# Optimization experiments

Hardware: AMD Instinct MI355X
Metric: run time of the kernel (lower is better)

## Reference

```python
import jax, jax.numpy as jnp
import numpy as np

N, E, D_IN, D_H, D_OUT, L = 100000, 1000000, 128, 64, 40, 7
MSG_EPS = 1e-7   # GENConv message epsilon
BN_EPS = 1e-5    # torch BatchNorm1d eps
T = 1.0          # softmax temperature (learn_t=False)


def _segment_softmax(logits, seg, n):
    # numerically stable softmax over edges grouped by destination node
    m = jax.ops.segment_max(logits, seg, num_segments=n)
    e = jnp.exp(logits - m[seg])
    s = jax.ops.segment_sum(e, seg, num_segments=n)
    return e / (s[seg] + 1e-16)


def _gen_conv(h, src, dst, W, b):
    # GENConv, aggr='softmax_sg', mlp_layers=1, msg_norm=False
    msg = jax.nn.relu(h[src]) + MSG_EPS                 # [E, D_H]
    w = jax.lax.stop_gradient(_segment_softmax(msg * T, dst, N))
    agg = jax.ops.segment_sum(w * msg, dst, num_segments=N)  # [N, D_H]
    return (h + agg) @ W + b


def _batch_norm(h, gamma, beta):
    mu = jnp.mean(h, axis=0)
    var = jnp.mean(jnp.square(h - mu), axis=0)  # biased var (training mode)
    return gamma * (h - mu) * jax.lax.rsqrt(var + BN_EPS) + beta


def setup_inputs() -> dict:
    key = jax.random.key(0)
    ks = jax.random.split(key, 6)
    x = jax.random.normal(ks[0], (N, D_IN), dtype=jnp.float32)
    edge_index = jax.random.randint(ks[1], (2, E), 0, N, dtype=jnp.int64)
    W_enc = jax.random.normal(ks[2], (D_IN, D_H), dtype=jnp.float32) / np.float32(np.sqrt(D_IN))
    b_enc = jnp.zeros((D_H,), jnp.float32)
    Wg = jax.random.normal(ks[3], (L, D_H, D_H), dtype=jnp.float32) / np.float32(np.sqrt(D_H))
    bg = jnp.zeros((L, D_H), jnp.float32)
    gamma = jnp.ones((L, D_H), jnp.float32)
    beta = jnp.zeros((L, D_H), jnp.float32)
    W_pred = jax.random.normal(ks[4], (D_H, D_OUT), dtype=jnp.float32) / np.float32(np.sqrt(D_H))
    b_pred = jnp.zeros((D_OUT,), jnp.float32)
    return {"x": x, "edge_index": edge_index, "W_enc": W_enc, "b_enc": b_enc,
            "Wg": Wg, "bg": bg, "gamma": gamma, "beta": beta,
            "W_pred": W_pred, "b_pred": b_pred}


def reference(x, edge_index, W_enc, b_enc, Wg, bg, gamma, beta, W_pred, b_pred):
    src, dst = edge_index[0], edge_index[1]
    h = x @ W_enc + b_enc                               # node encoder
    h = _gen_conv(h, src, dst, Wg[0], bg[0])            # first conv (res+)
    for layer in range(1, L):                            # BN->ReLU->Conv->Res
        h2 = jax.nn.relu(_batch_norm(h, gamma[layer - 1], beta[layer - 1]))
        h = _gen_conv(h2, src, dst, Wg[layer], bg[layer]) + h
    h = jax.nn.relu(_batch_norm(h, gamma[L - 1], beta[L - 1]))
    logits = h @ W_pred + b_pred
    return jax.nn.log_softmax(logits, axis=-1)
```

## Files before the change

kernel.cpp:

```cpp
#include <hip/hip_runtime.h>
#include <math.h>

#define NN 100000
#define NE 1000000
#define DH 64
#define DIN 128
#define DOUT 40
#define NL 7
#define SCAN_B 1024
#define NBLK ((NN + SCAN_B - 1) / SCAN_B)
#define NGRP (NN / 16)
#define LBLK ((NGRP + 3) / 4)
#define COLB_CAP (NE + 8 * NN + 64)
#define QS 16.0f
#define IQS 0.0625f

typedef _Float16 v8h __attribute__((ext_vector_type(8)));
typedef float v4f __attribute__((ext_vector_type(4)));

__global__ __launch_bounds__(256) void k_count4(const int* __restrict__ dst,
                                                int* __restrict__ cnt4,
                                                int* __restrict__ pi) {
  int i = blockIdx.x * 256 + threadIdx.x;
  if (i < NE) pi[i] = atomicAdd(&cnt4[(size_t)(i & 3) * NN + dst[i]], 1);
}

__global__ __launch_bounds__(SCAN_B) void k_scan1(const int* __restrict__ cnt4,
                                                  int* __restrict__ cnt,
                                                  int* __restrict__ rp8,
                                                  int* __restrict__ rp8s,
                                                  int* __restrict__ bsum) {
  __shared__ int buf[SCAN_B];
  int i = blockIdx.x * SCAN_B + threadIdx.x;
  int c0 = 0, c1 = 0, c2 = 0, c3 = 0;
  if (i < NN) {
    c0 = cnt4[i];
    c1 = cnt4[(size_t)NN + i];
    c2 = cnt4[(size_t)2 * NN + i];
    c3 = cnt4[(size_t)3 * NN + i];
  }
  int tot = c0 + c1 + c2 + c3;
  int t8 = (tot + 7) & ~7;
  buf[threadIdx.x] = t8;
  __syncthreads();
  for (int off = 1; off < SCAN_B; off <<= 1) {
    int t = (threadIdx.x >= off) ? buf[threadIdx.x - off] : 0;
    __syncthreads();
    buf[threadIdx.x] += t;
    __syncthreads();
  }
  if (i < NN) {
    int excl = buf[threadIdx.x] - t8;
    cnt[i] = tot;
    rp8[i] = excl;
    rp8s[4 * i] = excl;
    rp8s[4 * i + 1] = excl + c0;
    rp8s[4 * i + 2] = excl + c0 + c1;
    rp8s[4 * i + 3] = excl + c0 + c1 + c2;
  }
  if (threadIdx.x == SCAN_B - 1) bsum[blockIdx.x] = buf[SCAN_B - 1];
}

__global__ __launch_bounds__(128) void k_scan2(int* __restrict__ bsum) {
  __shared__ int buf[128];
  int v = (threadIdx.x < NBLK) ? bsum[threadIdx.x] : 0;
  buf[threadIdx.x] = v;
  __syncthreads();
  for (int off = 1; off < 128; off <<= 1) {
    int t = (threadIdx.x >= off) ? buf[threadIdx.x - off] : 0;
    __syncthreads();
    buf[threadIdx.x] += t;
    __syncthreads();
  }
  if (threadIdx.x < NBLK) bsum[threadIdx.x] = buf[threadIdx.x] - v;
}

__global__ __launch_bounds__(SCAN_B) void k_scan3(int* __restrict__ rp8,
                                                  int* __restrict__ rp8s,
                                                  const int* __restrict__ bsum) {
  int i = blockIdx.x * SCAN_B + threadIdx.x;
  if (i < NN) {
    int b = bsum[blockIdx.x];
    rp8[i] += b;
    rp8s[4 * i] += b;
    rp8s[4 * i + 1] += b;
    rp8s[4 * i + 2] += b;
    rp8s[4 * i + 3] += b;
  }
}

__global__ __launch_bounds__(256) void k_place(const int* __restrict__ src,
                                               const int* __restrict__ dst,
                                               const int* __restrict__ rp8s,
                                               const int* __restrict__ pi,
                                               int* __restrict__ colb) {
  int i = blockIdx.x * 256 + threadIdx.x;
  if (i < NE)
    colb[rp8s[4 * dst[i] + (i & 3)] + pi[i]] = src[i] * DH + DH;
}

__global__ __launch_bounds__(256) void k_enc_mfma(const float* __restrict__ x,
                                                  const float* __restrict__ W,
                                                  const float* __restrict__ b,
                                                  float* __restrict__ h) {
  __shared__ _Float16 Atile[4][2048];
  const int tid = threadIdx.x;
  const int w = tid >> 6, lane = tid & 63;
  const int gid = blockIdx.x * 4 + w;
  if (gid >= NGRP) return;
  const int row = lane & 15, hi = lane >> 4;

  v8h bf[4][4];
#pragma unroll
  for (int kt = 0; kt < 4; ++kt)
#pragma unroll
    for (int ct = 0; ct < 4; ++ct)
#pragma unroll
      for (int j = 0; j < 8; ++j)
        bf[kt][ct][j] = (_Float16)W[(kt * 32 + hi * 8 + j) * DH + ct * 16 + row];

  const int base = gid * 16;
  _Float16* At = &Atile[w][0];
#pragma unroll 4
  for (int i = 0; i < 16; ++i) {
    float v0 = x[(size_t)(base + i) * DIN + lane];
    float v1 = x[(size_t)(base + i) * DIN + 64 + lane];
    int swi = (i & 7) << 4;
    At[(i * 256 + ((lane * 2) ^ swi)) >> 1] = (_Float16)v0;
    At[(i * 256 + 128 + ((lane * 2) ^ swi)) >> 1] = (_Float16)v1;
  }
  const int sw = (row & 7) << 4;
  v8h a[4];
#pragma unroll
  for (int kt = 0; kt < 4; ++kt) {
    int off = (kt & 1) * 64 + hi * 16;
    a[kt] = *(const v8h*)&At[(row * 256 + (kt >> 1) * 128 + (off ^ sw)) >> 1];
  }
  v4f c0 = {0, 0, 0, 0}, c1 = {0, 0, 0, 0}, c2 = {0, 0, 0, 0}, c3 = {0, 0, 0, 0};
#pragma unroll
  for (int kt = 0; kt < 4; ++kt) {
    c0 = __builtin_amdgcn_mfma_f32_16x16x32_f16(a[kt], bf[kt][0], c0, 0, 0, 0);
    c1 = __builtin_amdgcn_mfma_f32_16x16x32_f16(a[kt], bf[kt][1], c1, 0, 0, 0);
    c2 = __builtin_amdgcn_mfma_f32_16x16x32_f16(a[kt], bf[kt][2], c2, 0, 0, 0);
    c3 = __builtin_amdgcn_mfma_f32_16x16x32_f16(a[kt], bf[kt][3], c3, 0, 0, 0);
  }
  float b0 = b[row], b1 = b[16 + row], b2 = b[32 + row], b3 = b[48 + row];
#pragma unroll
  for (int reg = 0; reg < 4; ++reg) {
    size_t o = (size_t)(base + hi * 4 + reg) * DH;
    h[o + row] = c0[reg] + b0;
    h[o + 16 + row] = c1[reg] + b1;
    h[o + 32 + row] = c2[reg] + b2;
    h[o + 48 + row] = c3[reg] + b3;
  }
}

__global__ __launch_bounds__(256) void k_msg(const float* __restrict__ h,
                                             const float* __restrict__ stats_in,
                                             const float* __restrict__ gamma,
                                             const float* __restrict__ beta,
                                             unsigned char* __restrict__ msg) {
  int lane = threadIdx.x & 63;
  float scale = 1.f, shift = 0.f;
  if (stats_in) {
    float mu = stats_in[lane] * (1.0f / NN);
    float var = stats_in[64 + lane] * (1.0f / NN) - mu * mu;
    scale = gamma[lane] * rsqrtf(var + 1e-5f);
    shift = beta[lane] - mu * scale;
  }
  int wid = (blockIdx.x * blockDim.x + threadIdx.x) >> 6;
  int nw = (gridDim.x * blockDim.x) >> 6;
  for (int n = wid; n < NN; n += nw) {
    float r = h[n * DH + lane];
    float v = fmaxf(fmaf(r, scale, shift), 0.f) + 1e-7f;
    msg[DH + n * DH + lane] = (unsigned char)fminf(v * QS + 0.5f, 255.f);
  }
}

__global__ __launch_bounds__(256, 8) void k_agg(const unsigned char* __restrict__ msg,
                                                const int* __restrict__ rp8,
                                                const int* __restrict__ cnt,
                                                const int* __restrict__ colb,
                                                _Float16* __restrict__ agg) {
  const int lane = threadIdx.x & 63;
  const int n = (blockIdx.x * 256 + threadIdx.x) >> 6;
  const int beg = __builtin_amdgcn_readfirstlane(rp8[n]);
  const int deg = __builtin_amdgcn_readfirstlane(cnt[n]);
  const int pdeg = (deg + 7) & ~7;
  const unsigned char* mb = msg + lane;
  float s = 0.f, t = 0.f;
  for (int j = 0; j < pdeg; j += 8) {
    int cc[8];
#pragma unroll
    for (int k = 0; k < 8; ++k) cc[k] = colb[beg + j + k];
    float vv[8];
#pragma unroll
    for (int k = 0; k < 8; ++k) vv[k] = (float)mb[cc[k]] * IQS;
#pragma unroll
    for (int k = 0; k < 8; ++k) {
      float e = __expf(vv[k]);
      s += e;
      t = fmaf(e, vv[k], t);
    }
  }
  s -= (float)(pdeg - deg);
  agg[(size_t)n * DH + lane] = (_Float16)(t / (s + 1e-16f));
}

__global__ __launch_bounds__(256) void k_mfma(
    const float* __restrict__ h_pre, const _Float16* __restrict__ agg,
    const float* __restrict__ stats_in,
    const float* __restrict__ gamma, const float* __restrict__ beta,
    const float* __restrict__ W, const float* __restrict__ b, int add_res,
    float* __restrict__ hout, float* __restrict__ partial) {
  __shared__ _Float16 Atile[4][1024];
  const int tid = threadIdx.x;
  const int w = tid >> 6, lane = tid & 63;
  const int gid = blockIdx.x * 4 + w;
  const int row = lane & 15, hi = lane >> 4;

  float ss0 = 0, ss1 = 0, ss2 = 0, ss3 = 0;
  float qq0 = 0, qq1 = 0, qq2 = 0, qq3 = 0;

  if (gid < NGRP) {
    float scale = 1.f, shift = 0.f;
    if (stats_in) {
      float mu = stats_in[lane] * (1.0f / NN);
      float var = stats_in[64 + lane] * (1.0f / NN) - mu * mu;
      scale = gamma[lane] * rsqrtf(var + 1e-5f);
      shift = beta[lane] - mu * scale;
    }
    v8h bf[2][4];
#pragma unroll
    for (int kt = 0; kt < 2; ++kt)
#pragma unroll
      for (int ct = 0; ct < 4; ++ct)
#pragma unroll
        for (int j = 0; j < 8; ++j)
          bf[kt][ct][j] = (_Float16)W[(kt * 32 + hi * 8 + j) * DH + ct * 16 + row];

    const int base = gid * 16;
    const float* hl = h_pre + lane;
    const _Float16* agl = agg + lane;
    _Float16* At = &Atile[w][0];

    float rawv[16], agv[16];
#pragma unroll
    for (int i = 0; i < 16; ++i) {
      size_t o = (size_t)(base + i) * DH;
      rawv[i] = hl[o];
      agv[i] = (float)agl[o];
    }
    float res[4][4];
    if (add_res) {
#pragma unroll
      for (int reg = 0; reg < 4; ++reg) {
        size_t o = (size_t)(base + hi * 4 + reg) * DH;
        res[reg][0] = h_pre[o + row];
        res[reg][1] = h_pre[o + 16 + row];
        res[reg][2] = h_pre[o + 32 + row];
        res[reg][3] = h_pre[o + 48 + row];
      }
    }
#pragma unroll
    for (int i = 0; i < 16; ++i) {
      float v = stats_in ? fmaxf(fmaf(rawv[i], scale, shift), 0.f) : rawv[i];
      v += agv[i];
      At[(i * 128 + ((lane * 2) ^ ((i & 7) << 4))) >> 1] = (_Float16)v;
    }
    const int sw = (row & 7) << 4;
    v8h a0 = *(const v8h*)&At[((row * 128) + ((hi * 16) ^ sw)) >> 1];
    v8h a1 = *(const v8h*)&At[((row * 128) + ((64 + hi * 16) ^ sw)) >> 1];
    v4f c0 = {0, 0, 0, 0}, c1 = {0, 0, 0, 0}, c2 = {0, 0, 0, 0}, c3 = {0, 0, 0, 0};
    c0 = __builtin_amdgcn_mfma_f32_16x16x32_f16(a0, bf[0][0], c0, 0, 0, 0);
    c0 = __builtin_amdgcn_mfma_f32_16x16x32_f16(a1, bf[1][0], c0, 0, 0, 0);
    c1 = __builtin_amdgcn_mfma_f32_16x16x32_f16(a0, bf[0][1], c1, 0, 0, 0);
    c1 = __builtin_amdgcn_mfma_f32_16x16x32_f16(a1, bf[1][1], c1, 0, 0, 0);
    c2 = __builtin_amdgcn_mfma_f32_16x16x32_f16(a0, bf[0][2], c2, 0, 0, 0);
    c2 = __builtin_amdgcn_mfma_f32_16x16x32_f16(a1, bf[1][2], c2, 0, 0, 0);
    c3 = __builtin_amdgcn_mfma_f32_16x16x32_f16(a0, bf[0][3], c3, 0, 0, 0);
    c3 = __builtin_amdgcn_mfma_f32_16x16x32_f16(a1, bf[1][3], c3, 0, 0, 0);

    float b0 = b[row], b1 = b[16 + row], b2 = b[32 + row], b3 = b[48 + row];
#pragma unroll
    for (int reg = 0; reg < 4; ++reg) {
      size_t o = (size_t)(base + hi * 4 + reg) * DH;
      float a0v = c0[reg] + b0;
      float a1v = c1[reg] + b1;
      float a2v = c2[reg] + b2;
      float a3v = c3[reg] + b3;
      if (add_res) {
        a0v += res[reg][0];
        a1v += res[reg][1];
        a2v += res[reg][2];
        a3v += res[reg][3];
      }
      hout[o + row] = a0v;
      hout[o + 16 + row] = a1v;
      hout[o + 32 + row] = a2v;
      hout[o + 48 + row] = a3v;
      ss0 += a0v; qq0 = fmaf(a0v, a0v, qq0);
      ss1 += a1v; qq1 = fmaf(a1v, a1v, qq1);
      ss2 += a2v; qq2 = fmaf(a2v, a2v, qq2);
      ss3 += a3v; qq3 = fmaf(a3v, a3v, qq3);
    }
  }

#pragma unroll
  for (int off = 16; off <= 32; off <<= 1) {
    ss0 += __shfl_xor(ss0, off, 64); ss1 += __shfl_xor(ss1, off, 64);
    ss2 += __shfl_xor(ss2, off, 64); ss3 += __shfl_xor(ss3, off, 64);
    qq0 += __shfl_xor(qq0, off, 64); qq1 += __shfl_xor(qq1, off, 64);
    qq2 += __shfl_xor(qq2, off, 64); qq3 += __shfl_xor(qq3, off, 64);
  }
  __syncthreads();
  float* Sr = (float*)&Atile[0][0];
  if (lane < 16) {
    Sr[w * 128 + lane] = ss0;       Sr[w * 128 + 16 + lane] = ss1;
    Sr[w * 128 + 32 + lane] = ss2;  Sr[w * 128 + 48 + lane] = ss3;
    Sr[w * 128 + 64 + lane] = qq0;  Sr[w * 128 + 80 + lane] = qq1;
    Sr[w * 128 + 96 + lane] = qq2;  Sr[w * 128 + 112 + lane] = qq3;
  }
  __syncthreads();
  if (tid < 128) {
    float vsum = Sr[tid] + Sr[128 + tid] + Sr[256 + tid] + Sr[384 + tid];
    partial[(size_t)blockIdx.x * 128 + tid] = vsum;
  }
}

__global__ __launch_bounds__(256) void k_red(const float* __restrict__ partial,
                                             float* __restrict__ stats) {
  const int f = blockIdx.x;
  float acc = 0.f;
  for (int i = threadIdx.x; i < LBLK; i += 256)
    acc += partial[(size_t)i * 128 + f];
  __shared__ float buf[256];
  buf[threadIdx.x] = acc;
  __syncthreads();
  for (int off = 128; off >= 1; off >>= 1) {
    if (threadIdx.x < off) buf[threadIdx.x] += buf[threadIdx.x + off];
    __syncthreads();
  }
  if (threadIdx.x == 0) stats[f] = buf[0];
}

__global__ __launch_bounds__(256) void k_pred_mfma(
    const float* __restrict__ h_pre, const float* __restrict__ stats_in,
    const float* __restrict__ gamma, const float* __restrict__ beta,
    const float* __restrict__ Wp, const float* __restrict__ bp,
    float* __restrict__ out) {
  __shared__ _Float16 Atile[4][1024];
  const int tid = threadIdx.x;
  const int w = tid >> 6, lane = tid & 63;
  const int gid = blockIdx.x * 4 + w;
  if (gid >= NGRP) return;
  const int row = lane & 15, hi = lane >> 4;

  float mu = stats_in[lane] * (1.0f / NN);
  float var = stats_in[64 + lane] * (1.0f / NN) - mu * mu;
  float scale = gamma[lane] * rsqrtf(var + 1e-5f);
  float shift = beta[lane] - mu * scale;

  v8h bf[2][3];
#pragma unroll
  for (int kt = 0; kt < 2; ++kt)
#pragma unroll
    for (int ct = 0; ct < 3; ++ct) {
      int n = ct * 16 + row;
#pragma unroll
      for (int j = 0; j < 8; ++j)
        bf[kt][ct][j] =
            (n < DOUT) ? (_Float16)Wp[(kt * 32 + hi * 8 + j) * DOUT + n]
                       : (_Float16)0.f;
    }

  const int base = gid * 16;
  const float* hl = h_pre + lane;
  _Float16* At = &Atile[w][0];
#pragma unroll 4
  for (int i = 0; i < 16; ++i) {
    float raw = hl[(size_t)(base + i) * DH];
    float v = fmaxf(fmaf(raw, scale, shift), 0.f);
    At[(i * 128 + ((lane * 2) ^ ((i & 7) << 4))) >> 1] = (_Float16)v;
  }
  const int sw = (row & 7) << 4;
  v8h a0 = *(const v8h*)&At[((row * 128) + ((hi * 16) ^ sw)) >> 1];
  v8h a1 = *(const v8h*)&At[((row * 128) + ((64 + hi * 16) ^ sw)) >> 1];
  v4f c0 = {0, 0, 0, 0}, c1 = {0, 0, 0, 0}, c2 = {0, 0, 0, 0};
  c0 = __builtin_amdgcn_mfma_f32_16x16x32_f16(a0, bf[0][0], c0, 0, 0, 0);
  c0 = __builtin_amdgcn_mfma_f32_16x16x32_f16(a1, bf[1][0], c0, 0, 0, 0);
  c1 = __builtin_amdgcn_mfma_f32_16x16x32_f16(a0, bf[0][1], c1, 0, 0, 0);
  c1 = __builtin_amdgcn_mfma_f32_16x16x32_f16(a1, bf[1][1], c1, 0, 0, 0);
  c2 = __builtin_amdgcn_mfma_f32_16x16x32_f16(a0, bf[0][2], c2, 0, 0, 0);
  c2 = __builtin_amdgcn_mfma_f32_16x16x32_f16(a1, bf[1][2], c2, 0, 0, 0);

  float bp0 = bp[row], bp1 = bp[16 + row];
  float bp2 = (32 + row < DOUT) ? bp[32 + row] : 0.f;
  bool v2 = (32 + row) < DOUT;
#pragma unroll
  for (int reg = 0; reg < 4; ++reg) {
    float l0 = c0[reg] + bp0;
    float l1 = c1[reg] + bp1;
    float l2 = v2 ? (c2[reg] + bp2) : -INFINITY;
    float xm = fmaxf(fmaxf(l0, l1), l2);
#pragma unroll
    for (int off = 1; off <= 8; off <<= 1) xm = fmaxf(xm, __shfl_xor(xm, off, 64));
    float e = __expf(l0 - xm) + __expf(l1 - xm) + (v2 ? __expf(l2 - xm) : 0.f);
#pragma unroll
    for (int off = 1; off <= 8; off <<= 1) e += __shfl_xor(e, off, 64);
    float ls = xm + __logf(e);
    size_t o = (size_t)(base + hi * 4 + reg) * DOUT;
    out[o + row] = l0 - ls;
    out[o + 16 + row] = l1 - ls;
    if (v2) out[o + 32 + row] = l2 - ls;
  }
}

extern "C" void kernel_launch(void* const* d_in, const int* in_sizes, int n_in,
                              void* d_out, int out_size, void* d_ws, size_t ws_size,
                              hipStream_t stream) {
  const float* x      = (const float*)d_in[0];
  const int*   ei     = (const int*)d_in[1];
  const float* W_enc  = (const float*)d_in[2];
  const float* b_enc  = (const float*)d_in[3];
  const float* Wg     = (const float*)d_in[4];
  const float* bg     = (const float*)d_in[5];
  const float* gamma  = (const float*)d_in[6];
  const float* beta   = (const float*)d_in[7];
  const float* W_pred = (const float*)d_in[8];
  const float* b_pred = (const float*)d_in[9];
  float* out = (float*)d_out;

  const int* src = ei;
  const int* dst = ei + NE;

  char* p = (char*)d_ws;
  auto alloc = [&](size_t bytes) -> void* {
    void* r = (void*)p;
    p += (bytes + 255) & ~(size_t)255;
    return r;
  };
  float*         hA      = (float*)alloc((size_t)NN * DH * 4);
  float*         hB      = (float*)alloc((size_t)NN * DH * 4);
  unsigned char* msg     = (unsigned char*)alloc((size_t)(NN + 1) * DH);
  _Float16*      agg     = (_Float16*)alloc((size_t)NN * DH * 2);
  int*           rp8     = (int*)alloc((size_t)NN * 4);
  int*           rp8s    = (int*)alloc((size_t)NN * 4 * 4);
  int*           pi      = (int*)alloc((size_t)NE * 4);
  int*           cnt     = (int*)alloc((size_t)NN * 4);
  int*           cnt4    = (int*)alloc((size_t)NN * 4 * 4);
  int*           colb    = (int*)alloc((size_t)COLB_CAP * 4);
  int*           bsum    = (int*)alloc((size_t)NBLK * 4);
  float*         stats   = (float*)alloc((size_t)NL * 128 * 4);
  float*         partial = (float*)alloc((size_t)LBLK * 128 * 4);

  hipMemsetAsync(cnt4, 0, (size_t)NN * 16, stream);
  hipMemsetAsync(colb, 0, (size_t)COLB_CAP * 4, stream);
  hipMemsetAsync(msg, 0, DH, stream);

  k_count4<<<(NE + 255) / 256, 256, 0, stream>>>(dst, cnt4, pi);
  k_scan1<<<NBLK, SCAN_B, 0, stream>>>(cnt4, cnt, rp8, rp8s, bsum);
  k_scan2<<<1, 128, 0, stream>>>(bsum);
  k_scan3<<<NBLK, SCAN_B, 0, stream>>>(rp8, rp8s, bsum);
  k_place<<<(NE + 255) / 256, 256, 0, stream>>>(src, dst, rp8s, pi, colb);

  k_enc_mfma<<<LBLK, 256, 0, stream>>>(x, W_enc, b_enc, hA);

  const int MSG_BLOCKS = 1024;
  const int AGG_BLOCKS = NN * 64 / 256;

  k_msg<<<MSG_BLOCKS, 256, 0, stream>>>(hA, nullptr, nullptr, nullptr, msg);
  k_agg<<<AGG_BLOCKS, 256, 0, stream>>>(msg, rp8, cnt, colb, agg);
  k_mfma<<<LBLK, 256, 0, stream>>>(
      hA, agg, nullptr, nullptr, nullptr, Wg, bg, 0, hB, partial);
  k_red<<<128, 256, 0, stream>>>(partial, stats);

  float* h = hB;
  float* hn = hA;
  for (int l = 1; l < NL; ++l) {
    const float* st = stats + (size_t)(l - 1) * 128;
    const float* g  = gamma + (size_t)(l - 1) * DH;
    const float* be = beta + (size_t)(l - 1) * DH;
    k_msg<<<MSG_BLOCKS, 256, 0, stream>>>(h, st, g, be, msg);
    k_agg<<<AGG_BLOCKS, 256, 0, stream>>>(msg, rp8, cnt, colb, agg);
    k_mfma<<<LBLK, 256, 0, stream>>>(
        h, agg, st, g, be,
        Wg + (size_t)l * DH * DH, bg + (size_t)l * DH, 1,
        hn, partial);
    k_red<<<128, 256, 0, stream>>>(partial, stats + (size_t)l * 128);
    float* tmp = h; h = hn; hn = tmp;
  }

  k_pred_mfma<<<LBLK, 256, 0, stream>>>(
      h, stats + (size_t)(NL - 1) * 128,
      gamma + (size_t)(NL - 1) * DH, beta + (size_t)(NL - 1) * DH,
      W_pred, b_pred, out);
}
```

Baseline: 517.5 us.

## Fuse softmax aggregation into MFMA layer kernel, dropping the fp16 agg buffer

Merges the per-node softmax aggregation kernel and the MFMA linear/residual/stats kernel into one kernel. Each block handles 16 nodes: every wave aggregates 4 nodes, writes the combined input tile to shared memory, then computes one 16-column slice of the output with MFMA. This removes the agg round-trip through global memory and one launch per layer. In exchange each block now does more serial gather work per wave, every block loads its slice of W, and the partial-stats buffer and k_red's reduction grow to one entry per 16 nodes.

Measured after the change: 525.2 us. Within noise of the previous version (+1.5%).

```diff
diff --git a/kernel.cpp b/kernel.cpp
--- a/kernel.cpp
+++ b/kernel.cpp
@@ -177,154 +177,88 @@
   }
 }
 
-__global__ __launch_bounds__(256, 8) void k_agg(const unsigned char* __restrict__ msg,
-                                                const int* __restrict__ rp8,
-                                                const int* __restrict__ cnt,
-                                                const int* __restrict__ colb,
-                                                _Float16* __restrict__ agg) {
-  const int lane = threadIdx.x & 63;
-  const int n = (blockIdx.x * 256 + threadIdx.x) >> 6;
-  const int beg = __builtin_amdgcn_readfirstlane(rp8[n]);
-  const int deg = __builtin_amdgcn_readfirstlane(cnt[n]);
-  const int pdeg = (deg + 7) & ~7;
-  const unsigned char* mb = msg + lane;
-  float s = 0.f, t = 0.f;
-  for (int j = 0; j < pdeg; j += 8) {
-    int cc[8];
-#pragma unroll
-    for (int k = 0; k < 8; ++k) cc[k] = colb[beg + j + k];
-    float vv[8];
-#pragma unroll
-    for (int k = 0; k < 8; ++k) vv[k] = (float)mb[cc[k]] * IQS;
-#pragma unroll
-    for (int k = 0; k < 8; ++k) {
-      float e = __expf(vv[k]);
-      s += e;
-      t = fmaf(e, vv[k], t);
-    }
-  }
-  s -= (float)(pdeg - deg);
-  agg[(size_t)n * DH + lane] = (_Float16)(t / (s + 1e-16f));
-}
-
-__global__ __launch_bounds__(256) void k_mfma(
-    const float* __restrict__ h_pre, const _Float16* __restrict__ agg,
-    const float* __restrict__ stats_in,
+__global__ __launch_bounds__(256) void k_layer2(
+    const float* __restrict__ h_pre, const unsigned char* __restrict__ msg,
+    const int* __restrict__ rp8, const int* __restrict__ cnt,
+    const int* __restrict__ colb, const float* __restrict__ stats_in,
     const float* __restrict__ gamma, const float* __restrict__ beta,
     const float* __restrict__ W, const float* __restrict__ b, int add_res,
     float* __restrict__ hout, float* __restrict__ partial) {
-  __shared__ _Float16 Atile[4][1024];
+  __shared__ _Float16 At[1024];
   const int tid = threadIdx.x;
   const int w = tid >> 6, lane = tid & 63;
-  const int gid = blockIdx.x * 4 + w;
   const int row = lane & 15, hi = lane >> 4;
-
-  float ss0 = 0, ss1 = 0, ss2 = 0, ss3 = 0;
-  float qq0 = 0, qq1 = 0, qq2 = 0, qq3 = 0;
-
-  if (gid < NGRP) {
-    float scale = 1.f, shift = 0.f;
-    if (stats_in) {
-      float mu = stats_in[lane] * (1.0f / NN);
-      float var = stats_in[64 + lane] * (1.0f / NN) - mu * mu;
-      scale = gamma[lane] * rsqrtf(var + 1e-5f);
-      shift = beta[lane] - mu * scale;
-    }
-    v8h bf[2][4];
-#pragma unroll
-    for (int kt = 0; kt < 2; ++kt)
-#pragma unroll
-      for (int ct = 0; ct < 4; ++ct)
-#pragma unroll
-        for (int j = 0; j < 8; ++j)
-          bf[kt][ct][j] = (_Float16)W[(kt * 32 + hi * 8 + j) * DH + ct * 16 + row];
-
-    const int base = gid * 16;
-    const float* hl = h_pre + lane;
-    const _Float16* agl = agg + lane;
-    _Float16* At = &Atile[w][0];
-
-    float rawv[16], agv[16];
-#pragma unroll
-    for (int i = 0; i < 16; ++i) {
-      size_t o = (size_t)(base + i) * DH;
-      rawv[i] = hl[o];
-      agv[i] = (float)agl[o];
-    }
-    float res[4][4];
-    if (add_res) {
-#pragma unroll
-      for (int reg = 0; reg < 4; ++reg) {
-        size_t o = (size_t)(base + hi * 4 + reg) * DH;
-        res[reg][0] = h_pre[o + row];
-        res[reg][1] = h_pre[o + 16 + row];
-        res[reg][2] = h_pre[o + 32 + row];
-        res[reg][3] = h_pre[o + 48 + row];
+  const int base = blockIdx.x * 16;
+
+  float scale = 1.f, shift = 0.f;
+  if (stats_in) {
+    float mu = stats_in[lane] * (1.0f / NN);
+    float var = stats_in[64 + lane] * (1.0f / NN) - mu * mu;
+    scale = gamma[lane] * rsqrtf(var + 1e-5f);
+    shift = beta[lane] - mu * scale;
+  }
+  v8h bf0, bf1;
+#pragma unroll
+  for (int j = 0; j < 8; ++j) {
+    bf0[j] = (_Float16)W[(hi * 8 + j) * DH + w * 16 + row];
+    bf1[j] = (_Float16)W[(32 + hi * 8 + j) * DH + w * 16 + row];
+  }
+
+  const unsigned char* mb = msg + lane;
+#pragma unroll
+  for (int k = 0; k < 4; ++k) {
+    int n = base + w * 4 + k;
+    int beg = __builtin_amdgcn_readfirstlane(rp8[n]);
+    int deg = __builtin_amdgcn_readfirstlane(cnt[n]);
+    int pdeg = (deg + 7) & ~7;
+    float s = 0.f, t = 0.f;
+    for (int j = 0; j < pdeg; j += 8) {
+      int cc[8];
+#pragma unroll
+      for (int q = 0; q < 8; ++q) cc[q] = colb[beg + j + q];
+      float vv[8];
+#pragma unroll
+      for (int q = 0; q < 8; ++q) vv[q] = (float)mb[cc[q]] * IQS;
+#pragma unroll
+      for (int q = 0; q < 8; ++q) {
+        float e = __expf(vv[q]);
+        s += e;
+        t = fmaf(e, vv[q], t);
       }
     }
-#pragma unroll
-    for (int i = 0; i < 16; ++i) {
-      float v = stats_in ? fmaxf(fmaf(rawv[i], scale, shift), 0.f) : rawv[i];
-      v += agv[i];
-      At[(i * 128 + ((lane * 2) ^ ((i & 7) << 4))) >> 1] = (_Float16)v;
-    }
-    const int sw = (row & 7) << 4;
-    v8h a0 = *(const v8h*)&At[((row * 128) + ((hi * 16) ^ sw)) >> 1];
-    v8h a1 = *(const v8h*)&At[((row * 128) + ((64 + hi * 16) ^ sw)) >> 1];
-    v4f c0 = {0, 0, 0, 0}, c1 = {0, 0, 0, 0}, c2 = {0, 0, 0, 0}, c3 = {0, 0, 0, 0};
-    c0 = __builtin_amdgcn_mfma_f32_16x16x32_f16(a0, bf[0][0], c0, 0, 0, 0);
-    c0 = __builtin_amdgcn_mfma_f32_16x16x32_f16(a1, bf[1][0], c0, 0, 0, 0);
-    c1 = __builtin_amdgcn_mfma_f32_16x16x32_f16(a0, bf[0][1], c1, 0, 0, 0);
-    c1 = __builtin_amdgcn_mfma_f32_16x16x32_f16(a1, bf[1][1], c1, 0, 0, 0);
-    c2 = __builtin_amdgcn_mfma_f32_16x16x32_f16(a0, bf[0][2], c2, 0, 0, 0);
-    c2 = __builtin_amdgcn_mfma_f32_16x16x32_f16(a1, bf[1][2], c2, 0, 0, 0);
-    c3 = __builtin_amdgcn_mfma_f32_16x16x32_f16(a0, bf[0][3], c3, 0, 0, 0);
-    c3 = __builtin_amdgcn_mfma_f32_16x16x32_f16(a1, bf[1][3], c3, 0, 0, 0);
-
-    float b0 = b[row], b1 = b[16 + row], b2 = b[32 + row], b3 = b[48 + row];
-#pragma unroll
-    for (int reg = 0; reg < 4; ++reg) {
-      size_t o = (size_t)(base + hi * 4 + reg) * DH;
-      float a0v = c0[reg] + b0;
-      float a1v = c1[reg] + b1;
-      float a2v = c2[reg] + b2;
-      float a3v = c3[reg] + b3;
-      if (add_res) {
-        a0v += res[reg][0];
-        a1v += res[reg][1];
-        a2v += res[reg][2];
-        a3v += res[reg][3];
-      }
-      hout[o + row] = a0v;
-      hout[o + 16 + row] = a1v;
-      hout[o + 32 + row] = a2v;
-      hout[o + 48 + row] = a3v;
-      ss0 += a0v; qq0 = fmaf(a0v, a0v, qq0);
-      ss1 += a1v; qq1 = fmaf(a1v, a1v, qq1);
-      ss2 += a2v; qq2 = fmaf(a2v, a2v, qq2);
-      ss3 += a3v; qq3 = fmaf(a3v, a3v, qq3);
-    }
-  }
-
-#pragma unroll
-  for (int off = 16; off <= 32; off <<= 1) {
-    ss0 += __shfl_xor(ss0, off, 64); ss1 += __shfl_xor(ss1, off, 64);
-    ss2 += __shfl_xor(ss2, off, 64); ss3 += __shfl_xor(ss3, off, 64);
-    qq0 += __shfl_xor(qq0, off, 64); qq1 += __shfl_xor(qq1, off, 64);
-    qq2 += __shfl_xor(qq2, off, 64); qq3 += __shfl_xor(qq3, off, 64);
+    s -= (float)(pdeg - deg);
+    float aggv = t / (s + 1e-16f);
+    float raw = h_pre[(size_t)n * DH + lane];
+    float v = stats_in ? fmaxf(fmaf(raw, scale, shift), 0.f) : raw;
+    v += aggv;
+    int i = w * 4 + k;
+    At[(i * 128 + ((lane * 2) ^ ((i & 7) << 4))) >> 1] = (_Float16)v;
   }
   __syncthreads();
-  float* Sr = (float*)&Atile[0][0];
-  if (lane < 16) {
-    Sr[w * 128 + lane] = ss0;       Sr[w * 128 + 16 + lane] = ss1;
-    Sr[w * 128 + 32 + lane] = ss2;  Sr[w * 128 + 48 + lane] = ss3;
-    Sr[w * 128 + 64 + lane] = qq0;  Sr[w * 128 + 80 + lane] = qq1;
-    Sr[w * 128 + 96 + lane] = qq2;  Sr[w * 128 + 112 + lane] = qq3;
-  }
-  __syncthreads();
-  if (tid < 128) {
-    float vsum = Sr[tid] + Sr[128 + tid] + Sr[256 + tid] + Sr[384 + tid];
-    partial[(size_t)blockIdx.x * 128 + tid] = vsum;
+
+  const int sw = (row & 7) << 4;
+  v8h a0 = *(const v8h*)&At[((row * 128) + ((hi * 16) ^ sw)) >> 1];
+  v8h a1 = *(const v8h*)&At[((row * 128) + ((64 + hi * 16) ^ sw)) >> 1];
+  v4f c = {0, 0, 0, 0};
+  c = __builtin_amdgcn_mfma_f32_16x16x32_f16(a0, bf0, c, 0, 0, 0);
+  c = __builtin_amdgcn_mfma_f32_16x16x32_f16(a1, bf1, c, 0, 0, 0);
+
+  float bb = b[w * 16 + row];
+  float ss = 0.f, qq = 0.f;
+#pragma unroll
+  for (int reg = 0; reg < 4; ++reg) {
+    size_t o = (size_t)(base + hi * 4 + reg) * DH + w * 16 + row;
+    float av = c[reg] + bb;
+    if (add_res) av += h_pre[o];
+    hout[o] = av;
+    ss += av;
+    qq = fmaf(av, av, qq);
+  }
+  ss += __shfl_xor(ss, 16, 64); qq += __shfl_xor(qq, 16, 64);
+  ss += __shfl_xor(ss, 32, 64); qq += __shfl_xor(qq, 32, 64);
+  if (hi == 0) {
+    partial[(size_t)blockIdx.x * 128 + w * 16 + row] = ss;
+    partial[(size_t)blockIdx.x * 128 + 64 + w * 16 + row] = qq;
   }
 }
 
@@ -332,7 +266,7 @@
                                              float* __restrict__ stats) {
   const int f = blockIdx.x;
   float acc = 0.f;
-  for (int i = threadIdx.x; i < LBLK; i += 256)
+  for (int i = threadIdx.x; i < NGRP; i += 256)
     acc += partial[(size_t)i * 128 + f];
   __shared__ float buf[256];
   buf[threadIdx.x] = acc;
@@ -443,7 +377,6 @@
   float*         hA      = (float*)alloc((size_t)NN * DH * 4);
   float*         hB      = (float*)alloc((size_t)NN * DH * 4);
   unsigned char* msg     = (unsigned char*)alloc((size_t)(NN + 1) * DH);
-  _Float16*      agg     = (_Float16*)alloc((size_t)NN * DH * 2);
   int*           rp8     = (int*)alloc((size_t)NN * 4);
   int*           rp8s    = (int*)alloc((size_t)NN * 4 * 4);
   int*           pi      = (int*)alloc((size_t)NE * 4);
@@ -452,7 +385,7 @@
   int*           colb    = (int*)alloc((size_t)COLB_CAP * 4);
   int*           bsum    = (int*)alloc((size_t)NBLK * 4);
   float*         stats   = (float*)alloc((size_t)NL * 128 * 4);
-  float*         partial = (float*)alloc((size_t)LBLK * 128 * 4);
+  float*         partial = (float*)alloc((size_t)NGRP * 128 * 4);
 
   hipMemsetAsync(cnt4, 0, (size_t)NN * 16, stream);
   hipMemsetAsync(colb, 0, (size_t)COLB_CAP * 4, stream);
@@ -467,12 +400,10 @@
   k_enc_mfma<<<LBLK, 256, 0, stream>>>(x, W_enc, b_enc, hA);
 
   const int MSG_BLOCKS = 1024;
-  const int AGG_BLOCKS = NN * 64 / 256;
 
   k_msg<<<MSG_BLOCKS, 256, 0, stream>>>(hA, nullptr, nullptr, nullptr, msg);
-  k_agg<<<AGG_BLOCKS, 256, 0, stream>>>(msg, rp8, cnt, colb, agg);
-  k_mfma<<<LBLK, 256, 0, stream>>>(
-      hA, agg, nullptr, nullptr, nullptr, Wg, bg, 0, hB, partial);
+  k_layer2<<<NGRP, 256, 0, stream>>>(
+      hA, msg, rp8, cnt, colb, nullptr, nullptr, nullptr, Wg, bg, 0, hB, partial);
   k_red<<<128, 256, 0, stream>>>(partial, stats);
 
   float* h = hB;
@@ -482,9 +413,8 @@
     const float* g  = gamma + (size_t)(l - 1) * DH;
     const float* be = beta + (size_t)(l - 1) * DH;
     k_msg<<<MSG_BLOCKS, 256, 0, stream>>>(h, st, g, be, msg);
-    k_agg<<<AGG_BLOCKS, 256, 0, stream>>>(msg, rp8, cnt, colb, agg);
-    k_mfma<<<LBLK, 256, 0, stream>>>(
-        h, agg, st, g, be,
+    k_layer2<<<NGRP, 256, 0, stream>>>(
+        h, msg, rp8, cnt, colb, st, g, be,
         Wg + (size_t)l * DH * DH, bg + (size_t)l * DH, 1,
         hn, partial);
     k_red<<<128, 256, 0, stream>>>(partial, stats + (size_t)l * 128);
```
